# Performance work log

Measured on AMD Instinct MI355X. Metric: run time of the kernel, lower is better.

Reference implementation:

```python
import jax, jax.numpy as jnp
import numpy as np

PADDING = 2
STRIDE = 1

def setup_inputs() -> dict:
    key = jax.random.key(0)
    k1, k2 = jax.random.split(key)
    X = jax.random.normal(k1, (32, 32, 128, 128), dtype=jnp.float32)  # NCHW
    K = jax.random.normal(k2, (64, 32, 5, 5), dtype=jnp.float32)     # OIHW
    return {"X": X, "K": K}

def reference(X, K):
    # Faithful to the naive loop: zero-pad by PADDING on H and W, then a
    # stride-STRIDE cross-correlation (slice * kernel).sum() per output pixel
    # and output channel -> exactly a standard conv2d with no bias.
    out = jax.lax.conv_general_dilated(
        X, K,
        window_strides=(STRIDE, STRIDE),
        padding=[(PADDING, PADDING), (PADDING, PADDING)],
        dimension_numbers=("NCHW", "OIHW", "NCHW"),
    )
    return out
```

## Files before the change

kernel.cpp:

```cpp
#include <hip/hip_runtime.h>


#define C_IN 32
#define H 128
#define W 128
#define O_CH 64
#define KS 5
#define PAD 2
#define XH 20
#define XW 20
#define NSHIFT 25
#define KSLICE_U4 256
#define KP_BYTES (NSHIFT * KSLICE_U4 * 16)
#define SX_CELLS (XH * 4 * XW)

typedef _Float16 f16x8 __attribute__((ext_vector_type(8)));
typedef float f32x4 __attribute__((ext_vector_type(4)));

union H8 { _Float16 h[8]; uint4 q; };

__global__ __launch_bounds__(256)
void pack_k_kernel(const float* __restrict__ K, uint4* __restrict__ Kp) {
    int t = blockIdx.x * 256 + threadIdx.x;
    int lp = t & 15;
    int g  = (t >> 4) & 3;
    int nf = (t >> 6) & 3;
    int s  = t >> 8;
    int oc = nf * 16 + lp;
    H8 u;
#pragma unroll
    for (int j = 0; j < 8; ++j)
        u.h[j] = (_Float16)K[(size_t)(oc * C_IN + g * 8 + j) * (KS * KS) + s];
    Kp[t] = u.q;
}

struct Bfrag { uint4 q[4]; };

template<bool USE_KP>
static __device__ __forceinline__ void load_b(const uint4* kp4, const float* K,
                                              int s, int lg, int lp, int lane_off,
                                              Bfrag& b) {
    if (USE_KP) {
#pragma unroll
        for (int nf = 0; nf < 4; ++nf)
            b.q[nf] = kp4[s * 256 + nf * 64 + lane_off];
    } else {
#pragma unroll
        for (int nf = 0; nf < 4; ++nf) {
            H8 u;
#pragma unroll
            for (int j = 0; j < 8; ++j)
                u.h[j] = (_Float16)K[(size_t)((nf * 16 + lp) * C_IN + lg * 8 + j) * (KS * KS) + s];
            b.q[nf] = u.q;
        }
    }
}

static __device__ __forceinline__ void do_shift(const unsigned short* sX, int s,
                                                int wv, int lg, int lp,
                                                const Bfrag& b, f32x4 acc[4][4]) {
    const int ky = s / KS, kx = s % KS;
    f16x8 ah[4];
#pragma unroll
    for (int mf = 0; mf < 4; ++mf) {
        int off = (((wv * 4 + mf + ky) * 4 + lg) * XW + kx + lp) * 8;
        ah[mf] = *(const f16x8*)&sX[off];
    }
#pragma unroll
    for (int mf = 0; mf < 4; ++mf)
#pragma unroll
        for (int nf = 0; nf < 4; ++nf)
            acc[mf][nf] = __builtin_amdgcn_mfma_f32_16x16x32_f16(
                ah[mf], *(const f16x8*)&b.q[nf], acc[mf][nf], 0, 0, 0);
}

template<bool USE_KP>
__global__ __launch_bounds__(256, 4)
void conv5x5_f16(const float* __restrict__ X, const float* __restrict__ K,
                 const uint4* __restrict__ kp4, float* __restrict__ out) {
    __shared__ __align__(16) unsigned short sX[SX_CELLS * 8];

    const int tid  = threadIdx.x;
    const int lane = tid & 63;
    const int wv   = tid >> 6;
    const int lg   = lane >> 4;
    const int lp   = lane & 15;
    const int lane_off = lg * 16 + lp;

    const int bid = (blockIdx.x & 7) * 256 + (blockIdx.x >> 3);
    const int n    = bid >> 6;
    const int tile = bid & 63;
    const int ty0  = (tile >> 3) * 16;
    const int tx0  = (tile & 7) * 16;

    const float* Xn = X + (size_t)n * C_IN * H * W;
    for (int i = tid; i < SX_CELLS; i += 256) {
        int x = i % XW;
        int t = i / XW;
        int g = t & 3;
        int y = t >> 2;
        int gx = tx0 + x - PAD;
        int gy = ty0 + y - PAD;
        bool inb = ((unsigned)gx < (unsigned)W) && ((unsigned)gy < (unsigned)H);
        const float* p = Xn + (size_t)(g * 8) * (H * W) + gy * W + gx;
        H8 u;
#pragma unroll
        for (int j = 0; j < 8; ++j)
            u.h[j] = (_Float16)(inb ? p[j * (H * W)] : 0.f);
        ((uint4*)sX)[i] = u.q;
    }

    f32x4 acc[4][4];
#pragma unroll
    for (int mf = 0; mf < 4; ++mf)
#pragma unroll
        for (int nf = 0; nf < 4; ++nf)
            acc[mf][nf] = (f32x4){0.f, 0.f, 0.f, 0.f};

    Bfrag b0, b1;
    load_b<USE_KP>(kp4, K, 0, lg, lp, lane_off, b0);

    __syncthreads();

#pragma unroll 1
    for (int s = 0; s < NSHIFT - 1; s += 2) {
        load_b<USE_KP>(kp4, K, s + 1, lg, lp, lane_off, b1);
        do_shift(sX, s, wv, lg, lp, b0, acc);
        load_b<USE_KP>(kp4, K, (s + 2 <= NSHIFT - 1) ? s + 2 : NSHIFT - 1, lg, lp, lane_off, b0);
        do_shift(sX, s + 1, wv, lg, lp, b1, acc);
    }
    do_shift(sX, NSHIFT - 1, wv, lg, lp, b0, acc);

#pragma unroll
    for (int mf = 0; mf < 4; ++mf) {
        int y = ty0 + wv * 4 + mf;
#pragma unroll
        for (int nf = 0; nf < 4; ++nf) {
            int oc = nf * 16 + lp;
            size_t idx = (((size_t)n * O_CH + oc) * H + y) * W + tx0 + lg * 4;
            *(float4*)&out[idx] = *(float4*)&acc[mf][nf];
        }
    }
}

extern "C" void kernel_launch(void* const* d_in, const int* in_sizes, int n_in,
                              void* d_out, int out_size, void* d_ws, size_t ws_size,
                              hipStream_t stream) {
    const float* X = (const float*)d_in[0];
    const float* K = (const float*)d_in[1];
    float* out = (float*)d_out;

    if (ws_size >= (size_t)KP_BYTES) {
        uint4* Kp = (uint4*)d_ws;
        pack_k_kernel<<<dim3(25), dim3(256), 0, stream>>>(K, Kp);
        conv5x5_f16<true><<<dim3(2048), dim3(256), 0, stream>>>(X, K, Kp, out);
    } else {
        conv5x5_f16<false><<<dim3(2048), dim3(256), 0, stream>>>(X, K, nullptr, out);
    }
}
```

Baseline: 256.6 us.

## Stage packed weight slices in LDS via double-buffered async global_load_lds chunks

```diff
diff --git a/kernel.cpp b/kernel.cpp
--- a/kernel.cpp
+++ b/kernel.cpp
@@ -10,8 +10,10 @@
 #define XH 20
 #define XW 20
 #define NSHIFT 25
+#define CHUNK 3
+#define NCHUNKS 9
 #define KSLICE_U4 256
-#define KP_BYTES (NSHIFT * KSLICE_U4 * 16)
+#define KP_ALLOC (27 * KSLICE_U4 * 16)
 #define SX_CELLS (XH * 4 * XW)
 
 typedef _Float16 f16x8 __attribute__((ext_vector_type(8)));
@@ -34,32 +36,16 @@
     Kp[t] = u.q;
 }
 
-struct Bfrag { uint4 q[4]; };
-
-template<bool USE_KP>
-static __device__ __forceinline__ void load_b(const uint4* kp4, const float* K,
-                                              int s, int lg, int lp, int lane_off,
-                                              Bfrag& b) {
-    if (USE_KP) {
+static __device__ __forceinline__ void do_shift(const unsigned short* sX,
+                                                const unsigned short* sKbuf,
+                                                int sc, int s, int wv, int lg,
+                                                int lp, int lane,
+                                                f32x4 acc[4][4]) {
+    const int ky = s / KS, kx = s % KS;
+    f16x8 bh[4];
 #pragma unroll
-        for (int nf = 0; nf < 4; ++nf)
-            b.q[nf] = kp4[s * 256 + nf * 64 + lane_off];
-    } else {
-#pragma unroll
-        for (int nf = 0; nf < 4; ++nf) {
-            H8 u;
-#pragma unroll
-            for (int j = 0; j < 8; ++j)
-                u.h[j] = (_Float16)K[(size_t)((nf * 16 + lp) * C_IN + lg * 8 + j) * (KS * KS) + s];
-            b.q[nf] = u.q;
-        }
-    }
-}
-
-static __device__ __forceinline__ void do_shift(const unsigned short* sX, int s,
-                                                int wv, int lg, int lp,
-                                                const Bfrag& b, f32x4 acc[4][4]) {
-    const int ky = s / KS, kx = s % KS;
+    for (int nf = 0; nf < 4; ++nf)
+        bh[nf] = *(const f16x8*)&sKbuf[(sc * 256 + nf * 64 + lane) * 8];
     f16x8 ah[4];
 #pragma unroll
     for (int mf = 0; mf < 4; ++mf) {
@@ -71,27 +57,35 @@
 #pragma unroll
         for (int nf = 0; nf < 4; ++nf)
             acc[mf][nf] = __builtin_amdgcn_mfma_f32_16x16x32_f16(
-                ah[mf], *(const f16x8*)&b.q[nf], acc[mf][nf], 0, 0, 0);
+                ah[mf], bh[nf], acc[mf][nf], 0, 0, 0);
 }
 
 template<bool USE_KP>
-__global__ __launch_bounds__(256, 4)
-void conv5x5_f16(const float* __restrict__ X, const float* __restrict__ K,
-                 const uint4* __restrict__ kp4, float* __restrict__ out) {
+__global__ __launch_bounds__(256, 3)
+void conv5x5_f16c(const float* __restrict__ X, const float* __restrict__ K,
+                  const uint4* __restrict__ kp4, float* __restrict__ out) {
     __shared__ __align__(16) unsigned short sX[SX_CELLS * 8];
+    __shared__ __align__(16) unsigned short sK[2][CHUNK * 2048];
 
     const int tid  = threadIdx.x;
     const int lane = tid & 63;
     const int wv   = tid >> 6;
     const int lg   = lane >> 4;
     const int lp   = lane & 15;
-    const int lane_off = lg * 16 + lp;
 
     const int bid = (blockIdx.x & 7) * 256 + (blockIdx.x >> 3);
     const int n    = bid >> 6;
     const int tile = bid & 63;
     const int ty0  = (tile >> 3) * 16;
     const int tx0  = (tile & 7) * 16;
+
+    if (USE_KP) {
+#pragma unroll
+        for (int j = 0; j < CHUNK; ++j)
+            __builtin_amdgcn_global_load_lds(
+                (const unsigned int*)(kp4 + tid + j * 256),
+                (unsigned int*)&((uint4*)sK[0])[tid + j * 256], 16, 0, 0);
+    }
 
     const float* Xn = X + (size_t)n * C_IN * H * W;
     for (int i = tid; i < SX_CELLS; i += 256) {
@@ -110,6 +104,22 @@
         ((uint4*)sX)[i] = u.q;
     }
 
+    if (!USE_KP) {
+#pragma unroll
+        for (int j = 0; j < CHUNK; ++j) {
+            int idx = tid + j * 256;
+            int s   = idx >> 8;
+            int nf  = (idx >> 6) & 3;
+            int l   = idx & 63;
+            H8 u;
+#pragma unroll
+            for (int jj = 0; jj < 8; ++jj)
+                u.h[jj] = (_Float16)K[(size_t)((nf * 16 + (l & 15)) * C_IN +
+                                               (l >> 4) * 8 + jj) * (KS * KS) + s];
+            ((uint4*)sK[0])[idx] = u.q;
+        }
+    }
+
     f32x4 acc[4][4];
 #pragma unroll
     for (int mf = 0; mf < 4; ++mf)
@@ -117,19 +127,48 @@
         for (int nf = 0; nf < 4; ++nf)
             acc[mf][nf] = (f32x4){0.f, 0.f, 0.f, 0.f};
 
-    Bfrag b0, b1;
-    load_b<USE_KP>(kp4, K, 0, lg, lp, lane_off, b0);
-
     __syncthreads();
 
 #pragma unroll 1
-    for (int s = 0; s < NSHIFT - 1; s += 2) {
-        load_b<USE_KP>(kp4, K, s + 1, lg, lp, lane_off, b1);
-        do_shift(sX, s, wv, lg, lp, b0, acc);
-        load_b<USE_KP>(kp4, K, (s + 2 <= NSHIFT - 1) ? s + 2 : NSHIFT - 1, lg, lp, lane_off, b0);
-        do_shift(sX, s + 1, wv, lg, lp, b1, acc);
+    for (int c = 0; c < NCHUNKS; ++c) {
+        const int cur = c & 1;
+
+        if (c < NCHUNKS - 1) {
+            if (USE_KP) {
+                const uint4* src = kp4 + (size_t)(c + 1) * (CHUNK * 256);
+#pragma unroll
+                for (int j = 0; j < CHUNK; ++j)
+                    __builtin_amdgcn_global_load_lds(
+                        (const unsigned int*)(src + tid + j * 256),
+                        (unsigned int*)&((uint4*)sK[cur ^ 1])[tid + j * 256], 16, 0, 0);
+            } else {
+#pragma unroll
+                for (int j = 0; j < CHUNK; ++j) {
+                    int idx = tid + j * 256;
+                    int s   = (c + 1) * CHUNK + (idx >> 8);
+                    if (s < NSHIFT) {
+                        int nf = (idx >> 6) & 3;
+                        int l  = idx & 63;
+                        H8 u;
+#pragma unroll
+                        for (int jj = 0; jj < 8; ++jj)
+                            u.h[jj] = (_Float16)K[(size_t)((nf * 16 + (l & 15)) * C_IN +
+                                                           (l >> 4) * 8 + jj) * (KS * KS) + s];
+                        ((uint4*)sK[cur ^ 1])[idx] = u.q;
+                    }
+                }
+            }
+        }
+
+#pragma unroll
+        for (int sc = 0; sc < CHUNK; ++sc) {
+            int s = c * CHUNK + sc;
+            if (s < NSHIFT)
+                do_shift(sX, sK[cur], sc, s, wv, lg, lp, lane, acc);
+        }
+
+        __syncthreads();
     }
-    do_shift(sX, NSHIFT - 1, wv, lg, lp, b0, acc);
 
 #pragma unroll
     for (int mf = 0; mf < 4; ++mf) {
@@ -150,11 +189,11 @@
     const float* K = (const float*)d_in[1];
     float* out = (float*)d_out;
 
-    if (ws_size >= (size_t)KP_BYTES) {
+    if (ws_size >= (size_t)KP_ALLOC) {
         uint4* Kp = (uint4*)d_ws;
         pack_k_kernel<<<dim3(25), dim3(256), 0, stream>>>(K, Kp);
-        conv5x5_f16<true><<<dim3(2048), dim3(256), 0, stream>>>(X, K, Kp, out);
+        conv5x5_f16c<true><<<dim3(2048), dim3(256), 0, stream>>>(X, K, Kp, out);
     } else {
-        conv5x5_f16<false><<<dim3(2048), dim3(256), 0, stream>>>(X, K, nullptr, out);
+        conv5x5_f16c<false><<<dim3(2048), dim3(256), 0, stream>>>(X, K, nullptr, out);
     }
 }
```

Result: slower. 283.2 us (+10.4%).
